# Kernel optimization log

Measured on AMD Instinct MI355X. Metric: run time of the kernel, lower is better.

Reference implementation:

```python
import jax, jax.numpy as jnp
from jax import lax
import numpy as np

N = 60000   # total nodes
B = 8       # graphs in batch
GS = N // B # nodes per graph
F = 384     # input node features
E = 600000  # edges
H = 6       # hiddenSize (hardcoded in source)
C = 10      # num_classes


def setup_inputs() -> dict:
    key = jax.random.key(0)
    ks = jax.random.split(key, 8)
    x = jax.random.normal(ks[0], (N, F), jnp.float32)
    src = jax.random.randint(ks[1], (E,), 0, N, jnp.int32)
    off = jax.random.randint(ks[2], (E,), 1, GS, jnp.int32)  # 1..GS-1 -> no self loops
    dst = (src // GS) * GS + (src % GS + off) % GS           # same-graph endpoint
    batch = jnp.arange(N, dtype=jnp.int32) // GS
    W1 = jax.random.normal(ks[3], (F, H), jnp.float32) * (1.0 / np.sqrt(F))
    b1 = jnp.zeros((H,), jnp.float32)
    W2 = jax.random.normal(ks[4], (H, C), jnp.float32) * (1.0 / np.sqrt(H))
    b2 = jnp.zeros((C,), jnp.float32)
    Wp1 = jax.random.normal(ks[5], (2 * H,), jnp.float32) * (1.0 / np.sqrt(2 * H))
    bp1 = jnp.zeros((), jnp.float32)
    Wp2 = jax.random.normal(ks[6], (2 * C,), jnp.float32) * (1.0 / np.sqrt(2 * C))
    bp2 = jnp.zeros((), jnp.float32)
    return dict(x=x, src=src, dst=dst, batch=batch, W1=W1, b1=b1, W2=W2, b2=b2,
                Wp1=Wp1, bp1=bp1, Wp2=Wp2, bp2=bp2)


def gcn_conv(x, src, dst, evalid, nvalid, W, b):
    # PyG GCNConv: h = x W; add remaining self-loops (weight 1); deg over dst;
    # norm = dinv[src]*dinv[dst]; aggregate to dst; + bias.
    n = x.shape[0]
    h = x @ W
    ef = evalid.astype(h.dtype)
    is_loop = evalid & (src == dst)
    has_loop = jax.ops.segment_sum(is_loop.astype(jnp.int32), dst, num_segments=n) > 0
    add_loop = (nvalid & ~has_loop).astype(h.dtype)
    deg = jax.ops.segment_sum(ef, dst, num_segments=n) + add_loop
    dinv = jnp.where(deg > 0, lax.rsqrt(jnp.maximum(deg, 1e-12)), 0.0)
    coef = ef * dinv[src] * dinv[dst]
    out = jax.ops.segment_sum(h[src] * coef[:, None], dst, num_segments=n)
    out = out + (add_loop * dinv * dinv)[:, None] * h
    return out + b


def edge_pool(x, src, dst, evalid, nvalid, Wp, bp):
    # PyG EdgePooling: raw = lin([x_src||x_dst]); score = softmax(raw, dst) + 0.5;
    # greedy contraction of edges by descending score; new_x = (sum over cluster) * score.
    n, f = x.shape
    raw = x[src] @ Wp[:f] + x[dst] @ Wp[f:] + bp                      # [E]
    rm = jnp.where(evalid, raw, -jnp.inf)
    m = jax.ops.segment_max(rm, dst, num_segments=n)
    m = jnp.where(jnp.isfinite(m), m, 0.0)
    ex = jnp.where(evalid, jnp.exp(raw - m[dst]), 0.0)
    s = jax.ops.segment_sum(ex, dst, num_segments=n)
    score = jnp.where(evalid, ex / jnp.where(s[dst] > 0, s[dst], 1.0), 0.0) + 0.5

    order = jnp.argsort(jnp.where(evalid, -score, jnp.inf))           # descending, invalid last

    def step(rem, edg):
        s_, d_, v_ = edg
        take = v_ & rem[s_] & rem[d_]
        rem = rem.at[s_].set(rem[s_] & ~take)
        rem = rem.at[d_].set(rem[d_] & ~take)
        return rem, take

    _, chosen_sorted = lax.scan(step, nvalid, (src[order], dst[order], evalid[order]))
    chosen = jnp.zeros_like(evalid).at[order].set(chosen_sorted)

    chf = chosen.astype(x.dtype)
    nonself = src != dst
    dead = jax.ops.segment_sum((chosen & nonself).astype(jnp.int32), dst, num_segments=n) > 0
    new_valid = nvalid & ~dead

    # merged feature: (x_src + x_dst) * score at slot src; unmatched: x * 1
    added = jnp.zeros_like(x).at[src].add((chf * nonself.astype(x.dtype))[:, None] * x[dst])
    scale = 1.0 + jnp.zeros((n,), x.dtype).at[src].add(chf * (score - 1.0))
    new_x = jnp.where(new_valid[:, None], (x + added) * scale[:, None], 0.0)

    # cluster map (dst of chosen edge -> src slot), remap + coalesce (dedup) edges
    merged_src = jnp.full((n,), -1, jnp.int32).at[dst].max(jnp.where(chosen, src, -1))
    cmap = jnp.where(merged_src >= 0, merged_src, jnp.arange(n, dtype=jnp.int32))
    ns, nd = cmap[src], cmap[dst]
    ns_k = jnp.where(evalid, ns, n)  # push invalid edges to the end
    order2 = jnp.lexsort((nd, ns_k))
    ss, dd = ns_k[order2], nd[order2]
    diff = (ss[1:] != ss[:-1]) | (dd[1:] != dd[:-1])
    first = jnp.concatenate([jnp.ones((1,), bool), diff])
    new_evalid = jnp.zeros_like(evalid).at[order2].set(first & evalid[order2])
    return new_x, ns, nd, new_evalid, new_valid


def _forward(x, src, dst, batch, W1, b1, W2, b2, Wp1, bp1, Wp2, bp2):
    evalid = jnp.ones((src.shape[0],), bool)
    nvalid = jnp.ones((x.shape[0],), bool)
    h = jax.nn.relu(gcn_conv(x, src, dst, evalid, nvalid, W1, b1))
    # dropout: identity in eval mode
    h, s1, d1, ev1, nv1 = edge_pool(h, src, dst, evalid, nvalid, Wp1, bp1)
    h = gcn_conv(h, s1, d1, ev1, nv1, W2, b2)
    h, s2, d2, ev2, nv2 = edge_pool(h, s1, d1, ev1, nv1, Wp2, bp2)
    nvf = nv2.astype(h.dtype)
    cnt = jax.ops.segment_sum(nvf, batch, num_segments=B)
    sm = jax.ops.segment_sum(h * nvf[:, None], batch, num_segments=B)
    g = sm / cnt[:, None]
    return jax.nn.log_softmax(g, axis=1)


def reference(x, src, dst, batch, W1, b1, W2, b2, Wp1, bp1, Wp2, bp2):
    return _forward(x, src, dst, batch, W1, b1, W2, b2, Wp1, bp1, Wp2, bp2)
```

## Files before the change

kernel.cpp:

```cpp
#include <hip/hip_runtime.h>
#include <math.h>

#define NN 60000
#define BB 8
#define GS 7500
#define FF 384
#define EE 600000
#define HH 6
#define CC 10
#define HT_BITS 20
#define HT_SIZE (1u << HT_BITS)
#define HT_MASK (HT_SIZE - 1u)
#define TPB 256
#define CAP 80000
#define REMW ((GS + 31) / 32)
#define GPAD 32
#define SCAN_B 1024
#define NBLK ((NN + SCAN_B - 1) / SCAN_B)
static_assert(NBLK <= 64, "scan2 assumes <=64 blocks");

static inline int ngrid(int n) { return (n + TPB - 1) / TPB; }

__device__ __forceinline__ unsigned long long mkprio(float sc, int e) {
  return (((unsigned long long)__float_as_uint(sc)) << 32) |
         (unsigned int)(~(unsigned int)e);
}

__global__ void k_mm1(const float* __restrict__ x, const float* __restrict__ W,
                      float* __restrict__ out) {
  __shared__ float Ws[FF * HH];
  for (int i = threadIdx.x; i < FF * HH; i += blockDim.x) Ws[i] = W[i];
  __syncthreads();
  int wave = threadIdx.x >> 6, lane = threadIdx.x & 63;
  int node = blockIdx.x * 4 + wave;
  if (node >= NN) return;
  const float* xr = x + (size_t)node * FF;
  float acc[HH] = {0.f, 0.f, 0.f, 0.f, 0.f, 0.f};
  for (int k = lane; k < FF; k += 64) {
    float xv = xr[k];
#pragma unroll
    for (int j = 0; j < HH; j++) acc[j] += xv * Ws[k * HH + j];
  }
#pragma unroll
  for (int j = 0; j < HH; j++) {
#pragma unroll
    for (int o = 32; o > 0; o >>= 1) acc[j] += __shfl_down(acc[j], o, 64);
  }
  if (lane == 0) {
#pragma unroll
    for (int j = 0; j < HH; j++) out[(size_t)node * HH + j] = acc[j];
  }
}

__global__ void k_prep(float* __restrict__ deg, unsigned char* __restrict__ hasloop,
                       int* __restrict__ gcntsA,
                       int* __restrict__ gcntsB, float* __restrict__ gsum,
                       float* __restrict__ gcnt, const unsigned char* __restrict__ nvin,
                       unsigned char* __restrict__ nvout, float* __restrict__ scale,
                       int* __restrict__ merged, int* __restrict__ partner,
                       unsigned long long* __restrict__ bestA,
                       unsigned long long* __restrict__ bestB,
                       unsigned char* __restrict__ remG) {
  int v = blockIdx.x * blockDim.x + threadIdx.x;
  if (v >= NN) return;
  deg[v] = 0.f;
  hasloop[v] = 0;
  unsigned char nvv = nvin ? nvin[v] : 1;
  nvout[v] = nvv;
  remG[v] = nvv;
  bestA[v] = 0ULL;
  bestB[v] = 0ULL;
  scale[v] = 1.0f;
  if (merged) merged[v] = -1;
  partner[v] = -1;
  if (v < BB * GPAD) { gcntsA[v] = 0; gcntsB[v] = 0; }
  if (v < BB * CC) gsum[v] = 0.f;
  if (v < BB) gcnt[v] = 0.f;
}

__global__ void k_deg(const int* __restrict__ src, const int* __restrict__ dst,
                      const unsigned char* __restrict__ ev, float* __restrict__ deg,
                      unsigned char* __restrict__ hasloop) {
  int e = blockIdx.x * blockDim.x + threadIdx.x;
  if (e >= EE) return;
  if (ev && !ev[e]) return;
  int d = dst[e];
  atomicAdd(&deg[d], 1.0f);
  if (src[e] == d) hasloop[d] = 1;
}

__global__ __launch_bounds__(1024) void k_scan1(const float* __restrict__ deg,
                                                int* __restrict__ rowstart,
                                                int* __restrict__ bsum) {
  __shared__ int tmp[SCAN_B];
  int t = threadIdx.x;
  int i = blockIdx.x * SCAN_B + t;
  int v = (i < NN) ? (int)deg[i] : 0;
  tmp[t] = v;
  __syncthreads();
  for (int o = 1; o < SCAN_B; o <<= 1) {
    int y = (t >= o) ? tmp[t - o] : 0;
    __syncthreads();
    tmp[t] += y;
    __syncthreads();
  }
  if (i < NN) rowstart[i] = tmp[t] - v;
  if (t == SCAN_B - 1) bsum[blockIdx.x] = tmp[t];
}

__global__ void k_scan2(int* __restrict__ bsum, int* __restrict__ rowstartNN) {
  int t = threadIdx.x;
  int v = (t < NBLK) ? bsum[t] : 0;
  int x = v;
#pragma unroll
  for (int o = 1; o < 64; o <<= 1) {
    int y = __shfl_up(x, o, 64);
    if (t >= o) x += y;
  }
  if (t < NBLK) bsum[t] = x - v;
  if (t == NBLK - 1) *rowstartNN = x;
}

__global__ void k_scan3(int* __restrict__ rowstart, const int* __restrict__ bsum,
                        int* __restrict__ fill, const float* __restrict__ deg,
                        const unsigned char* __restrict__ hasloop,
                        const unsigned char* __restrict__ nv, float* __restrict__ dinv,
                        unsigned char* __restrict__ addloop) {
  int i = blockIdx.x * blockDim.x + threadIdx.x;
  if (i >= NN) return;
  int r = rowstart[i] + bsum[i >> 10];
  rowstart[i] = r;
  fill[i] = r;
  int nvv = nv ? (int)nv[i] : 1;
  unsigned char al = (nvv && !hasloop[i]) ? 1 : 0;
  float d = deg[i] + (float)al;
  dinv[i] = d > 0.f ? 1.0f / sqrtf(fmaxf(d, 1e-12f)) : 0.f;
  addloop[i] = al;
}

__global__ void k_scatter(const int* __restrict__ src, const int* __restrict__ dst,
                          const unsigned char* __restrict__ ev, int* __restrict__ fill,
                          int* __restrict__ csrS, int* __restrict__ csrE) {
  int e = blockIdx.x * blockDim.x + threadIdx.x;
  if (e >= EE) return;
  if (ev && !ev[e]) return;
  int d = dst[e];
  int p = atomicAdd(&fill[d], 1);
  csrS[p] = src[e];
  csrE[p] = e;
}

template <int FD>
__global__ void k_agg_fin(const int* __restrict__ rowstart, const int* __restrict__ csrS,
                          const float* __restrict__ dinv, const unsigned char* __restrict__ addloop,
                          const float* __restrict__ h, const float* __restrict__ b,
                          float* __restrict__ out, int relu) {
  int v = blockIdx.x * blockDim.x + threadIdx.x;
  if (v >= NN) return;
  int b0 = rowstart[v], b1 = rowstart[v + 1];
  float acc[FD];
#pragma unroll
  for (int j = 0; j < FD; j++) acc[j] = 0.f;
  float dv = dinv[v];
  for (int i = b0; i < b1; i++) {
    int s = csrS[i];
    float c = dinv[s] * dv;
    const float* hr = h + (size_t)s * FD;
#pragma unroll
    for (int j = 0; j < FD; j++) acc[j] += hr[j] * c;
  }
  float cl = addloop[v] ? dv * dv : 0.f;
  const float* hv = h + (size_t)v * FD;
#pragma unroll
  for (int j = 0; j < FD; j++) {
    float o = acc[j] + cl * hv[j] + b[j];
    if (relu) o = fmaxf(o, 0.f);
    out[(size_t)v * FD + j] = o;
  }
}

__global__ void k_raw(const float* __restrict__ x, const int* __restrict__ src,
                      const int* __restrict__ dst, const unsigned char* __restrict__ ev,
                      const float* __restrict__ Wp, const float* __restrict__ bp,
                      float* __restrict__ raw, int fd) {
  int e = blockIdx.x * blockDim.x + threadIdx.x;
  if (e >= EE) return;
  if (ev && !ev[e]) return;
  int s = src[e], d = dst[e];
  float r = bp[0];
  for (int j = 0; j < fd; j++) r += x[(size_t)s * fd + j] * Wp[j];
  for (int j = 0; j < fd; j++) r += x[(size_t)d * fd + j] * Wp[fd + j];
  raw[e] = r;
}

__global__ void k_smscore(const int* __restrict__ rowstart, const int* __restrict__ csrS,
                          const int* __restrict__ csrE, const float* __restrict__ raw,
                          const unsigned char* __restrict__ remG, float* __restrict__ score,
                          unsigned long long* __restrict__ bestA) {
  int v = blockIdx.x * blockDim.x + threadIdx.x;
  if (v >= NN) return;
  int b0 = rowstart[v], b1 = rowstart[v + 1];
  if (b0 == b1) return;
  float m = -INFINITY;
  for (int i = b0; i < b1; i++) m = fmaxf(m, raw[csrE[i]]);
  float s = 0.f;
  for (int i = b0; i < b1; i++) s += expf(raw[csrE[i]] - m);
  if (!remG[v]) return;
  float sd = s > 0.f ? s : 1.0f;
  unsigned long long lb = 0ULL;
  for (int i = b0; i < b1; i++) {
    int sv = csrS[i];
    if (!remG[sv]) continue;
    int e = csrE[i];
    float sc = expf(raw[e] - m) / sd + 0.5f;
    score[e] = sc;
    unsigned long long p = mkprio(sc, e);
    if (p > lb) lb = p;
    if (sv != v && p > bestA[sv]) atomicMax(&bestA[sv], p);
  }
  if (lb > bestA[v]) atomicMax(&bestA[v], lb);
}

__global__ void k_r1sel(const int* __restrict__ src, const int* __restrict__ dst,
                        const float* __restrict__ score, const unsigned char* __restrict__ ev,
                        unsigned char* __restrict__ remG,
                        const unsigned long long* __restrict__ bestA,
                        unsigned long long* __restrict__ bestB,
                        unsigned char* __restrict__ chosen, ulonglong2* __restrict__ recs,
                        int* __restrict__ gcnts) {
  __shared__ int wcnt[TPB / 64][BB];
  __shared__ int bbase[BB];
  int e = blockIdx.x * blockDim.x + threadIdx.x;
  int w = threadIdx.x >> 6, lane = threadIdx.x & 63;
  int keep = 0, s = 0, d = 0, g = 0;
  unsigned long long p = 0;
  if (e < EE && (!ev || ev[e])) {
    s = src[e];
    d = dst[e];
    g = s / GS;
    if (remG[s] && remG[d]) {
      p = mkprio(score[e], e);
      if (bestA[s] == p && bestA[d] == p) {
        chosen[e] = 1;
        remG[s] = 0;
        remG[d] = 0;
      } else {
        keep = 1;
        bestB[s] = 0ULL;
        bestB[d] = 0ULL;
      }
    }
  }
  int myrank = 0;
#pragma unroll
  for (int gg = 0; gg < BB; gg++) {
    unsigned long long m = __ballot(keep && g == gg);
    if (keep && g == gg) myrank = __popcll(m & ((1ULL << lane) - 1ULL));
    if (lane == 0) wcnt[w][gg] = __popcll(m);
  }
  __syncthreads();
  if (threadIdx.x < BB) {
    int gg = threadIdx.x, tot = 0;
#pragma unroll
    for (int ww = 0; ww < TPB / 64; ww++) {
      int c = wcnt[ww][gg];
      wcnt[ww][gg] = tot;
      tot += c;
    }
    bbase[gg] = tot ? atomicAdd(&gcnts[gg * GPAD], tot) : 0;
  }
  __syncthreads();
  if (keep)
    recs[(size_t)g * CAP + bbase[g] + wcnt[w][g] + myrank] =
        make_ulonglong2(p, (((unsigned long long)(unsigned int)s) << 32) | (unsigned int)d);
}

__global__ void k_gpost(const ulonglong2* __restrict__ recs, const int* __restrict__ gcnts,
                        const unsigned char* __restrict__ remG,
                        unsigned long long* __restrict__ bestC, int* __restrict__ gcntsOut) {
  int g = blockIdx.y;
  if (blockIdx.x == 0 && threadIdx.x == 0) gcntsOut[g * GPAD] = 0;
  int n = gcnts[g * GPAD];
  const ulonglong2* lst = recs + (size_t)g * CAP;
  int stride = gridDim.x * blockDim.x;
  for (int i = blockIdx.x * blockDim.x + threadIdx.x; i < n; i += stride) {
    ulonglong2 r = lst[i];
    int s = (int)(r.y >> 32), d = (int)(r.y & 0xFFFFFFFFu);
    if (remG[s] && remG[d]) {
      if (r.x > bestC[s]) atomicMax(&bestC[s], r.x);
      if (d != s && r.x > bestC[d]) atomicMax(&bestC[d], r.x);
    }
  }
}

__global__ void k_gsel(const ulonglong2* __restrict__ recsIn, const int* __restrict__ gcntsIn,
                       unsigned char* __restrict__ remG,
                       const unsigned long long* __restrict__ bestC,
                       unsigned long long* __restrict__ bestN,
                       unsigned char* __restrict__ chosen, ulonglong2* __restrict__ recsOut,
                       int* __restrict__ gcntsOut) {
  int g = blockIdx.y;
  int n = gcntsIn[g * GPAD];
  const ulonglong2* lst = recsIn + (size_t)g * CAP;
  ulonglong2* outl = recsOut + (size_t)g * CAP;
  int lane = threadIdx.x & 63;
  int stride = gridDim.x * blockDim.x;
  for (int i = blockIdx.x * blockDim.x + threadIdx.x; i - lane < n; i += stride) {
    int keep = 0;
    ulonglong2 r;
    if (i < n) {
      r = lst[i];
      int s = (int)(r.y >> 32), d = (int)(r.y & 0xFFFFFFFFu);
      if (remG[s] && remG[d]) {
        if (bestC[s] == r.x && bestC[d] == r.x) {
          int e = (int)(~(unsigned int)(r.x & 0xFFFFFFFFu));
          chosen[e] = 1;
          remG[s] = 0;
          remG[d] = 0;
        } else {
          keep = 1;
          bestN[s] = 0ULL;
          bestN[d] = 0ULL;
        }
      }
    }
    unsigned long long m = __ballot(keep);
    int tot = __popcll(m);
    int pre = __popcll(m & ((1ULL << lane) - 1ULL));
    int b0 = 0;
    if (lane == 0 && tot) b0 = atomicAdd(&gcntsOut[g * GPAD], tot);
    b0 = __shfl(b0, 0, 64);
    if (keep) outl[b0 + pre] = r;
  }
}

__global__ __launch_bounds__(1024) void k_match_g(ulonglong2* __restrict__ recs0,
                                                  ulonglong2* __restrict__ recs1,
                                                  const int* __restrict__ gcnts,
                                                  const unsigned char* __restrict__ remG,
                                                  unsigned char* __restrict__ chosen) {
  __shared__ unsigned long long best[GS];
  __shared__ unsigned int remB[REMW];
  __shared__ int cnt_next;
  const int g = blockIdx.x;
  const int base = g * GS;
  const int t = threadIdx.x, nth = blockDim.x;
  const int lane = t & 63;

  for (int w = t; w < REMW; w += nth) {
    unsigned int bits = 0;
    int v0 = w * 32;
    if (v0 + 32 <= GS) {
      const unsigned int* p4 = (const unsigned int*)(remG + base + v0);
#pragma unroll
      for (int q = 0; q < 8; q++) {
        unsigned int x4 = p4[q];
        bits |= ((x4 & 1u) << (q * 4)) | (((x4 >> 8) & 1u) << (q * 4 + 1)) |
                (((x4 >> 16) & 1u) << (q * 4 + 2)) | (((x4 >> 24) & 1u) << (q * 4 + 3));
      }
    } else {
      for (int b = 0; b < 32; b++) {
        int v = v0 + b;
        if (v < GS) bits |= (remG[base + v] ? 1u : 0u) << b;
      }
    }
    remB[w] = bits;
  }
  for (int i = t; i < GS; i += nth) best[i] = 0ULL;
  __syncthreads();

  ulonglong2* bufs[2] = {recs0 + (size_t)g * CAP, recs1 + (size_t)g * CAP};
  int n = gcnts[g * GPAD];
  int cur = 0;
  int guard = 0;

  while (n > 0) {
    if (++guard > 100000) break;
    for (int i0 = 0; i0 < n; i0 += nth * 4) {
      ulonglong2 r[4];
      int have[4];
#pragma unroll
      for (int k = 0; k < 4; k++) {
        int i = i0 + t + k * nth;
        have[k] = i < n;
        if (have[k]) r[k] = bufs[cur][i];
      }
#pragma unroll
      for (int k = 0; k < 4; k++) {
        if (!have[k]) continue;
        int ls = (int)(r[k].y >> 32) - base, ld = (int)(r[k].y & 0xFFFFFFFFu) - base;
        if (((remB[ls >> 5] >> (ls & 31)) & 1u) && ((remB[ld >> 5] >> (ld & 31)) & 1u)) {
          atomicMax(&best[ls], r[k].x);
          if (ld != ls) atomicMax(&best[ld], r[k].x);
        }
      }
    }
    if (t == 0) cnt_next = 0;
    __syncthreads();
    for (int i0 = 0; i0 < n; i0 += nth * 4) {
      ulonglong2 r[4];
      int have[4];
#pragma unroll
      for (int k = 0; k < 4; k++) {
        int i = i0 + t + k * nth;
        have[k] = i < n;
        if (have[k]) r[k] = bufs[cur][i];
      }
#pragma unroll
      for (int k = 0; k < 4; k++) {
        int keep = 0;
        int ls = 0, ld = 0;
        if (have[k]) {
          ls = (int)(r[k].y >> 32) - base;
          ld = (int)(r[k].y & 0xFFFFFFFFu) - base;
          if (((remB[ls >> 5] >> (ls & 31)) & 1u) && ((remB[ld >> 5] >> (ld & 31)) & 1u)) {
            if (best[ls] == r[k].x && best[ld] == r[k].x) {
              int e = (int)(~(unsigned int)(r[k].x & 0xFFFFFFFFu));
              chosen[e] = 1;
              atomicAnd(&remB[ls >> 5], ~(1u << (ls & 31)));
              atomicAnd(&remB[ld >> 5], ~(1u << (ld & 31)));
            } else {
              keep = 1;
            }
          }
        }
        unsigned long long m = __ballot(keep);
        int tot = __popcll(m);
        int pre = __popcll(m & ((1ULL << lane) - 1ULL));
        int b0 = 0;
        if (lane == 0 && tot) b0 = atomicAdd(&cnt_next, tot);
        b0 = __shfl(b0, 0, 64);
        if (keep) bufs[cur ^ 1][b0 + pre] = r[k];
      }
    }
    __syncthreads();
    n = cnt_next;
    if (n < 4096) {
      for (int i = t; i < n; i += nth) {
        ulonglong2 r = bufs[cur ^ 1][i];
        best[(int)(r.y >> 32) - base] = 0ULL;
        best[(int)(r.y & 0xFFFFFFFFu) - base] = 0ULL;
      }
    } else {
      for (int i = t; i < GS; i += nth) best[i] = 0ULL;
    }
    __syncthreads();
    cur ^= 1;
  }
}

__global__ void k_pool_edge(const int* __restrict__ src, const int* __restrict__ dst,
                            const unsigned char* __restrict__ chosen, const float* __restrict__ score,
                            unsigned char* __restrict__ nvout, float* __restrict__ scale,
                            int* __restrict__ partner, int* __restrict__ merged) {
  int e = blockIdx.x * blockDim.x + threadIdx.x;
  if (e >= EE) return;
  if (!chosen[e]) return;
  int s = src[e], d = dst[e];
  scale[s] = score[e];
  if (merged) merged[d] = s;
  if (s != d) {
    nvout[d] = 0;
    partner[s] = d;
  }
}

__global__ void k_newx_mm2(const float* __restrict__ h1, const int* __restrict__ partner,
                           const float* __restrict__ scale, const unsigned char* __restrict__ nvout,
                           const float* __restrict__ W2, float* __restrict__ h2pre) {
  int v = blockIdx.x * blockDim.x + threadIdx.x;
  if (v >= NN) return;
  float sc = scale[v];
  int ok = nvout[v];
  int p = partner[v];
  float nx[HH];
#pragma unroll
  for (int j = 0; j < HH; j++) {
    float a = h1[(size_t)v * HH + j];
    if (p >= 0) a += h1[(size_t)p * HH + j];
    nx[j] = ok ? a * sc : 0.f;
  }
#pragma unroll
  for (int c = 0; c < CC; c++) {
    float a = 0.f;
#pragma unroll
    for (int j = 0; j < HH; j++) a += nx[j] * W2[j * CC + c];
    h2pre[(size_t)v * CC + c] = a;
  }
}

__device__ __forceinline__ unsigned int ht_hash(unsigned long long key) {
  return (unsigned int)((key * 0x9E3779B97F4A7C15ULL) >> 44) & HT_MASK;
}

__global__ void k_remap_ins(const int* __restrict__ src, const int* __restrict__ dst,
                            const int* __restrict__ merged, int* __restrict__ ns,
                            int* __restrict__ nd, unsigned long long* __restrict__ htab) {
  int e = blockIdx.x * blockDim.x + threadIdx.x;
  if (e >= EE) return;
  int s = src[e], d = dst[e];
  int ms = merged[s], md = merged[d];
  int a = ms >= 0 ? ms : s;
  int b = md >= 0 ? md : d;
  ns[e] = a;
  nd[e] = b;
  unsigned long long key =
      (unsigned long long)((((unsigned int)a) << 16) | (unsigned int)b);
  unsigned long long val = (key << 32) | (unsigned int)e;
  unsigned int h = ht_hash(key);
  for (;;) {
    unsigned long long curv = htab[h];
    if (curv == ~0ULL) {
      unsigned long long prev = atomicCAS(&htab[h], ~0ULL, val);
      if (prev == ~0ULL) break;
      curv = prev;
    }
    if ((curv >> 32) == key) {
      if ((curv & 0xFFFFFFFFULL) > (unsigned long long)(unsigned int)e)
        atomicMin(&htab[h], val);
      break;
    }
    h = (h + 1) & HT_MASK;
  }
}

__global__ void k_dedup_mark(const int* __restrict__ ns, const int* __restrict__ nd,
                             const unsigned long long* __restrict__ htab,
                             unsigned char* __restrict__ evout) {
  int e = blockIdx.x * blockDim.x + threadIdx.x;
  if (e >= EE) return;
  unsigned long long key =
      (unsigned long long)((((unsigned int)ns[e]) << 16) | (unsigned int)nd[e]);
  unsigned int h = ht_hash(key);
  for (;;) {
    unsigned long long curv = htab[h];
    if ((curv >> 32) == key) {
      evout[e] = ((curv & 0xFFFFFFFFULL) == (unsigned long long)(unsigned int)e) ? 1 : 0;
      return;
    }
    h = (h + 1) & HT_MASK;
  }
}

__global__ void k_newx_pool(const float* __restrict__ h2, const int* __restrict__ partner,
                            const float* __restrict__ scale, const unsigned char* __restrict__ nv,
                            float* __restrict__ gsum, float* __restrict__ gcnt) {
  int v = blockIdx.x * blockDim.x + threadIdx.x;
  int lane = threadIdx.x & 63;
  int b = (v < NN ? v : NN - 1) / GS;
  int active = (v < NN) && nv[v];
  float cnt = active ? 1.f : 0.f;
  float val[CC];
  if (active) {
    float sc = scale[v];
    int p = partner[v];
    for (int j = 0; j < CC; j++) {
      float a = h2[(size_t)v * CC + j];
      if (p >= 0) a += h2[(size_t)p * CC + j];
      val[j] = a * sc;
    }
  } else {
    for (int j = 0; j < CC; j++) val[j] = 0.f;
  }
  int b0 = __shfl(b, 0, 64);
  unsigned long long same = __ballot(b == b0);
  if (same == ~0ULL) {
    for (int o = 32; o > 0; o >>= 1) {
      cnt += __shfl_down(cnt, o, 64);
      for (int j = 0; j < CC; j++) val[j] += __shfl_down(val[j], o, 64);
    }
    if (lane == 0 && cnt > 0.f) {
      atomicAdd(&gcnt[b0], cnt);
      for (int j = 0; j < CC; j++) atomicAdd(&gsum[b0 * CC + j], val[j]);
    }
  } else if (active) {
    atomicAdd(&gcnt[b], cnt);
    for (int j = 0; j < CC; j++) atomicAdd(&gsum[b * CC + j], val[j]);
  }
}

__global__ void k_logsm(const float* __restrict__ gsum, const float* __restrict__ gcnt,
                        float* __restrict__ out) {
  int t = threadIdx.x;
  if (t >= BB) return;
  float gr[CC];
  float c = gcnt[t];
  float m = -INFINITY;
  for (int j = 0; j < CC; j++) {
    gr[j] = gsum[t * CC + j] / c;
    m = fmaxf(m, gr[j]);
  }
  float s = 0.f;
  for (int j = 0; j < CC; j++) s += expf(gr[j] - m);
  float l = logf(s);
  for (int j = 0; j < CC; j++) out[t * CC + j] = gr[j] - m - l;
}

extern "C" void kernel_launch(void* const* d_in, const int* in_sizes, int n_in,
                              void* d_out, int out_size, void* d_ws, size_t ws_size,
                              hipStream_t stream) {
  const float* x = (const float*)d_in[0];
  const int* src = (const int*)d_in[1];
  const int* dst = (const int*)d_in[2];
  const float* W1 = (const float*)d_in[4];
  const float* b1 = (const float*)d_in[5];
  const float* W2 = (const float*)d_in[6];
  const float* b2 = (const float*)d_in[7];
  const float* Wp1 = (const float*)d_in[8];
  const float* bp1 = (const float*)d_in[9];
  const float* Wp2 = (const float*)d_in[10];
  const float* bp2 = (const float*)d_in[11];
  float* out = (float*)d_out;

  char* wsb = (char*)d_ws;
  size_t off = 0;
  auto A = [&](size_t bytes) -> char* {
    char* r = wsb + off;
    off = (off + bytes + 255) & ~(size_t)255;
    return r;
  };
  float* h1pre = (float*)A((size_t)NN * HH * 4);
  float* h1out = (float*)A((size_t)NN * HH * 4);
  float* deg = (float*)A((size_t)NN * 4);
  float* dinv = (float*)A((size_t)NN * 4);
  unsigned char* hasloop = (unsigned char*)A(NN);
  unsigned char* addloop = (unsigned char*)A(NN);
  float* raw = (float*)A((size_t)EE * 4);
  float* score = (float*)A((size_t)EE * 4);
  unsigned char* chosen = (unsigned char*)A(EE);
  unsigned char* nv1 = (unsigned char*)A(NN);
  unsigned char* nv2 = (unsigned char*)A(NN);
  float* scale = (float*)A((size_t)NN * 4);
  int* partner = (int*)A((size_t)NN * 4);
  int* merged = (int*)A((size_t)NN * 4);
  int* ns = (int*)A((size_t)EE * 4);
  int* nd = (int*)A((size_t)EE * 4);
  unsigned char* ev1 = (unsigned char*)A(EE);
  unsigned long long* htab = (unsigned long long*)A((size_t)HT_SIZE * 8);
  float* h2pre = (float*)A((size_t)NN * CC * 4);
  float* h2out = (float*)A((size_t)NN * CC * 4);
  unsigned long long* bestA = (unsigned long long*)A((size_t)NN * 8);
  unsigned long long* bestB = (unsigned long long*)A((size_t)NN * 8);
  unsigned char* remG = (unsigned char*)A(NN);
  ulonglong2* recs0 = (ulonglong2*)A((size_t)BB * CAP * 16);
  ulonglong2* recs1 = (ulonglong2*)A((size_t)BB * CAP * 16);
  int* gcntsA = (int*)A((size_t)BB * GPAD * 4);
  int* gcntsB = (int*)A((size_t)BB * GPAD * 4);
  float* gsum = (float*)A((size_t)BB * CC * 4);
  float* gcnt = (float*)A((size_t)BB * 4);
  int* rowstart = (int*)A((size_t)(NN + 1) * 4);
  int* fill = (int*)A((size_t)NN * 4);
  int* bsum = (int*)A((size_t)64 * 4);
  int* csrS = (int*)A((size_t)EE * 4);
  int* csrE = (int*)A((size_t)EE * 4);
  (void)ws_size; (void)n_in; (void)in_sizes; (void)out_size;

  const int GE = ngrid(EE), GN = ngrid(NN);
  const dim3 RG(32, BB);

  hipMemsetAsync(htab, 0xFF, (size_t)HT_SIZE * 8, stream);
  hipLaunchKernelGGL(k_mm1, dim3((NN + 3) / 4), dim3(TPB), 0, stream, x, W1, h1pre);
  hipLaunchKernelGGL(k_prep, dim3(GN), dim3(TPB), 0, stream, deg, hasloop, gcntsA, gcntsB,
                     gsum, gcnt, (const unsigned char*)nullptr, nv1, scale, merged, partner, bestA, bestB, remG);
  hipLaunchKernelGGL(k_deg, dim3(GE), dim3(TPB), 0, stream, src, dst, (const unsigned char*)nullptr, deg, hasloop);
  hipLaunchKernelGGL(k_scan1, dim3(NBLK), dim3(SCAN_B), 0, stream, deg, rowstart, bsum);
  hipLaunchKernelGGL(k_scan2, dim3(1), dim3(64), 0, stream, bsum, rowstart + NN);
  hipLaunchKernelGGL(k_scan3, dim3(GN), dim3(TPB), 0, stream, rowstart, bsum, fill, deg, hasloop,
                     (const unsigned char*)nullptr, dinv, addloop);
  hipLaunchKernelGGL(k_scatter, dim3(GE), dim3(TPB), 0, stream, src, dst, (const unsigned char*)nullptr, fill, csrS, csrE);
  hipLaunchKernelGGL(k_agg_fin<HH>, dim3(GN), dim3(TPB), 0, stream, rowstart, csrS, dinv, addloop, h1pre, b1, h1out, 1);

  hipLaunchKernelGGL(k_raw, dim3(GE), dim3(TPB), 0, stream, h1out, src, dst, (const unsigned char*)nullptr, Wp1, bp1, raw, HH);
  hipMemsetAsync(chosen, 0, (size_t)EE, stream);
  hipLaunchKernelGGL(k_smscore, dim3(GN), dim3(TPB), 0, stream, rowstart, csrS, csrE, raw, remG, score, bestA);
  hipLaunchKernelGGL(k_r1sel, dim3(GE), dim3(TPB), 0, stream, src, dst, score, (const unsigned char*)nullptr, remG, bestA, bestB, chosen, recs0, gcntsA);
  hipLaunchKernelGGL(k_gpost, RG, dim3(TPB), 0, stream, recs0, gcntsA, remG, bestB, gcntsB);
  hipLaunchKernelGGL(k_gsel, RG, dim3(TPB), 0, stream, recs0, gcntsA, remG, bestB, bestA, chosen, recs1, gcntsB);
  hipLaunchKernelGGL(k_gpost, RG, dim3(TPB), 0, stream, recs1, gcntsB, remG, bestA, gcntsA);
  hipLaunchKernelGGL(k_gsel, RG, dim3(TPB), 0, stream, recs1, gcntsB, remG, bestA, bestB, chosen, recs0, gcntsA);
  hipLaunchKernelGGL(k_gpost, RG, dim3(TPB), 0, stream, recs0, gcntsA, remG, bestB, gcntsB);
  hipLaunchKernelGGL(k_gsel, RG, dim3(TPB), 0, stream, recs0, gcntsA, remG, bestB, bestA, chosen, recs1, gcntsB);
  hipLaunchKernelGGL(k_gpost, RG, dim3(TPB), 0, stream, recs1, gcntsB, remG, bestA, gcntsA);
  hipLaunchKernelGGL(k_gsel, RG, dim3(TPB), 0, stream, recs1, gcntsB, remG, bestA, bestB, chosen, recs0, gcntsA);
  hipLaunchKernelGGL(k_gpost, RG, dim3(TPB), 0, stream, recs0, gcntsA, remG, bestB, gcntsB);
  hipLaunchKernelGGL(k_gsel, RG, dim3(TPB), 0, stream, recs0, gcntsA, remG, bestB, bestA, chosen, recs1, gcntsB);
  hipLaunchKernelGGL(k_match_g, dim3(BB), dim3(1024), 0, stream, recs1, recs0, gcntsB, remG, chosen);
  hipLaunchKernelGGL(k_pool_edge, dim3(GE), dim3(TPB), 0, stream, src, dst, chosen, score, nv1, scale, partner, merged);
  hipLaunchKernelGGL(k_newx_mm2, dim3(GN), dim3(TPB), 0, stream, h1out, partner, scale, nv1, W2, h2pre);
  hipLaunchKernelGGL(k_remap_ins, dim3(GE), dim3(TPB), 0, stream, src, dst, merged, ns, nd, htab);
  hipLaunchKernelGGL(k_dedup_mark, dim3(GE), dim3(TPB), 0, stream, ns, nd, htab, ev1);

  hipLaunchKernelGGL(k_prep, dim3(GN), dim3(TPB), 0, stream, deg, hasloop, gcntsA, gcntsB,
                     gsum, gcnt, (const unsigned char*)nv1, nv2, scale, (int*)nullptr, partner, bestA, bestB, remG);
  hipLaunchKernelGGL(k_deg, dim3(GE), dim3(TPB), 0, stream, ns, nd, (const unsigned char*)ev1, deg, hasloop);
  hipLaunchKernelGGL(k_scan1, dim3(NBLK), dim3(SCAN_B), 0, stream, deg, rowstart, bsum);
  hipLaunchKernelGGL(k_scan2, dim3(1), dim3(64), 0, stream, bsum, rowstart + NN);
  hipLaunchKernelGGL(k_scan3, dim3(GN), dim3(TPB), 0, stream, rowstart, bsum, fill, deg, hasloop,
                     (const unsigned char*)nv1, dinv, addloop);
  hipLaunchKernelGGL(k_scatter, dim3(GE), dim3(TPB), 0, stream, ns, nd, (const unsigned char*)ev1, fill, csrS, csrE);
  hipLaunchKernelGGL(k_agg_fin<CC>, dim3(GN), dim3(TPB), 0, stream, rowstart, csrS, dinv, addloop, h2pre, b2, h2out, 0);

  hipLaunchKernelGGL(k_raw, dim3(GE), dim3(TPB), 0, stream, h2out, ns, nd, (const unsigned char*)ev1, Wp2, bp2, raw, CC);
  hipMemsetAsync(chosen, 0, (size_t)EE, stream);
  hipLaunchKernelGGL(k_smscore, dim3(GN), dim3(TPB), 0, stream, rowstart, csrS, csrE, raw, remG, score, bestA);
  hipLaunchKernelGGL(k_r1sel, dim3(GE), dim3(TPB), 0, stream, ns, nd, score, (const unsigned char*)ev1, remG, bestA, bestB, chosen, recs0, gcntsA);
  hipLaunchKernelGGL(k_gpost, RG, dim3(TPB), 0, stream, recs0, gcntsA, remG, bestB, gcntsB);
  hipLaunchKernelGGL(k_gsel, RG, dim3(TPB), 0, stream, recs0, gcntsA, remG, bestB, bestA, chosen, recs1, gcntsB);
  hipLaunchKernelGGL(k_gpost, RG, dim3(TPB), 0, stream, recs1, gcntsB, remG, bestA, gcntsA);
  hipLaunchKernelGGL(k_gsel, RG, dim3(TPB), 0, stream, recs1, gcntsB, remG, bestA, bestB, chosen, recs0, gcntsA);
  hipLaunchKernelGGL(k_gpost, RG, dim3(TPB), 0, stream, recs0, gcntsA, remG, bestB, gcntsB);
  hipLaunchKernelGGL(k_gsel, RG, dim3(TPB), 0, stream, recs0, gcntsA, remG, bestB, bestA, chosen, recs1, gcntsB);
  hipLaunchKernelGGL(k_gpost, RG, dim3(TPB), 0, stream, recs1, gcntsB, remG, bestA, gcntsA);
  hipLaunchKernelGGL(k_gsel, RG, dim3(TPB), 0, stream, recs1, gcntsB, remG, bestA, bestB, chosen, recs0, gcntsA);
  hipLaunchKernelGGL(k_gpost, RG, dim3(TPB), 0, stream, recs0, gcntsA, remG, bestB, gcntsB);
  hipLaunchKernelGGL(k_gsel, RG, dim3(TPB), 0, stream, recs0, gcntsA, remG, bestB, bestA, chosen, recs1, gcntsB);
  hipLaunchKernelGGL(k_match_g, dim3(BB), dim3(1024), 0, stream, recs1, recs0, gcntsB, remG, chosen);
  hipLaunchKernelGGL(k_pool_edge, dim3(GE), dim3(TPB), 0, stream, ns, nd, chosen, score, nv2, scale, partner, (int*)nullptr);

  hipLaunchKernelGGL(k_newx_pool, dim3(GN), dim3(TPB), 0, stream, h2out, partner, scale, nv2, gsum, gcnt);
  hipLaunchKernelGGL(k_logsm, dim3(1), dim3(64), 0, stream, gsum, gcnt, out);
}
```

Measured before the change: 1.469 ms.

## Fuse greedy-matching post/select rounds via round-tagged priorities and fold scan2 into scan3

Puts a round number into the high bits of each best-priority value, so each round can publish next-round maxima while it selects, without resetting arrays. This merges the separate post and select kernels into one k_gselpost per round, using three rotating counters. Also folds the single-block scan2 into scan3 (each block redoes the 64-entry wave scan) and moves clearing of the chosen array into k_raw instead of a memset. The goal is fewer launches and fewer passes over the record lists, at the cost of packing score bits and edge index into 51 bits, which assumes fewer than 2^20 edges.

New measurement: 1.707 ms. 1.16x slower.

```diff
diff --git a/kernel.cpp b/kernel.cpp
--- a/kernel.cpp
+++ b/kernel.cpp
@@ -17,13 +17,18 @@
 #define GPAD 32
 #define SCAN_B 1024
 #define NBLK ((NN + SCAN_B - 1) / SCAN_B)
-static_assert(NBLK <= 64, "scan2 assumes <=64 blocks");
+static_assert(NBLK <= 64, "scan3 wave-scan assumes <=64 blocks");
+static_assert(EE < (1 << 20), "tag tie-break assumes e < 2^20");
 
 static inline int ngrid(int n) { return (n + TPB - 1) / TPB; }
 
 __device__ __forceinline__ unsigned long long mkprio(float sc, int e) {
   return (((unsigned long long)__float_as_uint(sc)) << 32) |
          (unsigned int)(~(unsigned int)e);
+}
+__device__ __forceinline__ unsigned long long mktag(unsigned long long round,
+                                                    unsigned long long prio) {
+  return (round << 51) | ((prio >> 32) << 20) | ((unsigned int)prio & 0xFFFFFu);
 }
 
 __global__ void k_mm1(const float* __restrict__ x, const float* __restrict__ W,
@@ -53,8 +58,8 @@
 }
 
 __global__ void k_prep(float* __restrict__ deg, unsigned char* __restrict__ hasloop,
-                       int* __restrict__ gcntsA,
-                       int* __restrict__ gcntsB, float* __restrict__ gsum,
+                       int* __restrict__ gcntsA, int* __restrict__ gcntsB,
+                       int* __restrict__ gcntsC, float* __restrict__ gsum,
                        float* __restrict__ gcnt, const unsigned char* __restrict__ nvin,
                        unsigned char* __restrict__ nvout, float* __restrict__ scale,
                        int* __restrict__ merged, int* __restrict__ partner,
@@ -73,7 +78,7 @@
   scale[v] = 1.0f;
   if (merged) merged[v] = -1;
   partner[v] = -1;
-  if (v < BB * GPAD) { gcntsA[v] = 0; gcntsB[v] = 0; }
+  if (v < BB * GPAD) { gcntsA[v] = 0; gcntsB[v] = 0; gcntsC[v] = 0; }
   if (v < BB * CC) gsum[v] = 0.f;
   if (v < BB) gcnt[v] = 0.f;
 }
@@ -108,29 +113,32 @@
   if (t == SCAN_B - 1) bsum[blockIdx.x] = tmp[t];
 }
 
-__global__ void k_scan2(int* __restrict__ bsum, int* __restrict__ rowstartNN) {
-  int t = threadIdx.x;
-  int v = (t < NBLK) ? bsum[t] : 0;
-  int x = v;
-#pragma unroll
-  for (int o = 1; o < 64; o <<= 1) {
-    int y = __shfl_up(x, o, 64);
-    if (t >= o) x += y;
-  }
-  if (t < NBLK) bsum[t] = x - v;
-  if (t == NBLK - 1) *rowstartNN = x;
-}
-
 __global__ void k_scan3(int* __restrict__ rowstart, const int* __restrict__ bsum,
                         int* __restrict__ fill, const float* __restrict__ deg,
                         const unsigned char* __restrict__ hasloop,
                         const unsigned char* __restrict__ nv, float* __restrict__ dinv,
                         unsigned char* __restrict__ addloop) {
-  int i = blockIdx.x * blockDim.x + threadIdx.x;
+  __shared__ int offs[64];
+  __shared__ int total;
+  int t = threadIdx.x;
+  if (t < 64) {
+    int v = (t < NBLK) ? bsum[t] : 0;
+    int x = v;
+#pragma unroll
+    for (int o = 1; o < 64; o <<= 1) {
+      int y = __shfl_up(x, o, 64);
+      if (t >= o) x += y;
+    }
+    offs[t] = x - v;
+    if (t == 63) total = x;
+  }
+  __syncthreads();
+  int i = blockIdx.x * blockDim.x + t;
   if (i >= NN) return;
-  int r = rowstart[i] + bsum[i >> 10];
+  int r = rowstart[i] + offs[i >> 10];
   rowstart[i] = r;
   fill[i] = r;
+  if (i == NN - 1) rowstart[NN] = total;
   int nvv = nv ? (int)nv[i] : 1;
   unsigned char al = (nvv && !hasloop[i]) ? 1 : 0;
   float d = deg[i] + (float)al;
@@ -182,9 +190,10 @@
 __global__ void k_raw(const float* __restrict__ x, const int* __restrict__ src,
                       const int* __restrict__ dst, const unsigned char* __restrict__ ev,
                       const float* __restrict__ Wp, const float* __restrict__ bp,
-                      float* __restrict__ raw, int fd) {
+                      float* __restrict__ raw, unsigned char* __restrict__ chosen, int fd) {
   int e = blockIdx.x * blockDim.x + threadIdx.x;
   if (e >= EE) return;
+  chosen[e] = 0;
   if (ev && !ev[e]) return;
   int s = src[e], d = dst[e];
   float r = bp[0];
@@ -216,9 +225,15 @@
     score[e] = sc;
     unsigned long long p = mkprio(sc, e);
     if (p > lb) lb = p;
-    if (sv != v && p > bestA[sv]) atomicMax(&bestA[sv], p);
-  }
-  if (lb > bestA[v]) atomicMax(&bestA[v], lb);
+    if (sv != v) {
+      unsigned long long t1 = mktag(1, p);
+      if (t1 > bestA[sv]) atomicMax(&bestA[sv], t1);
+    }
+  }
+  if (lb) {
+    unsigned long long t1 = mktag(1, lb);
+    if (t1 > bestA[v]) atomicMax(&bestA[v], t1);
+  }
 }
 
 __global__ void k_r1sel(const int* __restrict__ src, const int* __restrict__ dst,
@@ -240,14 +255,16 @@
     g = s / GS;
     if (remG[s] && remG[d]) {
       p = mkprio(score[e], e);
-      if (bestA[s] == p && bestA[d] == p) {
+      unsigned long long t1 = mktag(1, p);
+      if (bestA[s] == t1 && bestA[d] == t1) {
         chosen[e] = 1;
         remG[s] = 0;
         remG[d] = 0;
       } else {
         keep = 1;
-        bestB[s] = 0ULL;
-        bestB[d] = 0ULL;
+        unsigned long long t2 = mktag(2, p);
+        atomicMax(&bestB[s], t2);
+        if (d != s) atomicMax(&bestB[d], t2);
       }
     }
   }
@@ -275,52 +292,37 @@
         make_ulonglong2(p, (((unsigned long long)(unsigned int)s) << 32) | (unsigned int)d);
 }
 
-__global__ void k_gpost(const ulonglong2* __restrict__ recs, const int* __restrict__ gcnts,
-                        const unsigned char* __restrict__ remG,
-                        unsigned long long* __restrict__ bestC, int* __restrict__ gcntsOut) {
+__global__ void k_gselpost(const ulonglong2* __restrict__ recsIn, const int* __restrict__ cntIn,
+                           unsigned char* __restrict__ remG,
+                           const unsigned long long* __restrict__ bestIn,
+                           unsigned long long* __restrict__ bestOut,
+                           unsigned char* __restrict__ chosen, ulonglong2* __restrict__ recsOut,
+                           int* __restrict__ cntOut, int* __restrict__ cntZero,
+                           unsigned long long rnd) {
   int g = blockIdx.y;
-  if (blockIdx.x == 0 && threadIdx.x == 0) gcntsOut[g * GPAD] = 0;
-  int n = gcnts[g * GPAD];
-  const ulonglong2* lst = recs + (size_t)g * CAP;
-  int stride = gridDim.x * blockDim.x;
-  for (int i = blockIdx.x * blockDim.x + threadIdx.x; i < n; i += stride) {
-    ulonglong2 r = lst[i];
-    int s = (int)(r.y >> 32), d = (int)(r.y & 0xFFFFFFFFu);
-    if (remG[s] && remG[d]) {
-      if (r.x > bestC[s]) atomicMax(&bestC[s], r.x);
-      if (d != s && r.x > bestC[d]) atomicMax(&bestC[d], r.x);
-    }
-  }
-}
-
-__global__ void k_gsel(const ulonglong2* __restrict__ recsIn, const int* __restrict__ gcntsIn,
-                       unsigned char* __restrict__ remG,
-                       const unsigned long long* __restrict__ bestC,
-                       unsigned long long* __restrict__ bestN,
-                       unsigned char* __restrict__ chosen, ulonglong2* __restrict__ recsOut,
-                       int* __restrict__ gcntsOut) {
-  int g = blockIdx.y;
-  int n = gcntsIn[g * GPAD];
+  if (blockIdx.x == 0 && threadIdx.x == 0) cntZero[g * GPAD] = 0;
+  int n = cntIn[g * GPAD];
   const ulonglong2* lst = recsIn + (size_t)g * CAP;
   ulonglong2* outl = recsOut + (size_t)g * CAP;
   int lane = threadIdx.x & 63;
   int stride = gridDim.x * blockDim.x;
   for (int i = blockIdx.x * blockDim.x + threadIdx.x; i - lane < n; i += stride) {
     int keep = 0;
+    int s = 0, d = 0;
     ulonglong2 r;
     if (i < n) {
       r = lst[i];
-      int s = (int)(r.y >> 32), d = (int)(r.y & 0xFFFFFFFFu);
+      s = (int)(r.y >> 32);
+      d = (int)(r.y & 0xFFFFFFFFu);
       if (remG[s] && remG[d]) {
-        if (bestC[s] == r.x && bestC[d] == r.x) {
+        unsigned long long tc = mktag(rnd, r.x);
+        if (bestIn[s] == tc && bestIn[d] == tc) {
           int e = (int)(~(unsigned int)(r.x & 0xFFFFFFFFu));
           chosen[e] = 1;
           remG[s] = 0;
           remG[d] = 0;
         } else {
           keep = 1;
-          bestN[s] = 0ULL;
-          bestN[d] = 0ULL;
         }
       }
     }
@@ -328,9 +330,14 @@
     int tot = __popcll(m);
     int pre = __popcll(m & ((1ULL << lane) - 1ULL));
     int b0 = 0;
-    if (lane == 0 && tot) b0 = atomicAdd(&gcntsOut[g * GPAD], tot);
+    if (lane == 0 && tot) b0 = atomicAdd(&cntOut[g * GPAD], tot);
     b0 = __shfl(b0, 0, 64);
-    if (keep) outl[b0 + pre] = r;
+    if (keep) {
+      outl[b0 + pre] = r;
+      unsigned long long tn = mktag(rnd + 1, r.x);
+      atomicMax(&bestOut[s], tn);
+      if (d != s) atomicMax(&bestOut[d], tn);
+    }
   }
 }
 
@@ -646,6 +653,7 @@
   ulonglong2* recs1 = (ulonglong2*)A((size_t)BB * CAP * 16);
   int* gcntsA = (int*)A((size_t)BB * GPAD * 4);
   int* gcntsB = (int*)A((size_t)BB * GPAD * 4);
+  int* gcntsC = (int*)A((size_t)BB * GPAD * 4);
   float* gsum = (float*)A((size_t)BB * CC * 4);
   float* gcnt = (float*)A((size_t)BB * 4);
   int* rowstart = (int*)A((size_t)(NN + 1) * 4);
@@ -660,61 +668,47 @@
 
   hipMemsetAsync(htab, 0xFF, (size_t)HT_SIZE * 8, stream);
   hipLaunchKernelGGL(k_mm1, dim3((NN + 3) / 4), dim3(TPB), 0, stream, x, W1, h1pre);
-  hipLaunchKernelGGL(k_prep, dim3(GN), dim3(TPB), 0, stream, deg, hasloop, gcntsA, gcntsB,
+  hipLaunchKernelGGL(k_prep, dim3(GN), dim3(TPB), 0, stream, deg, hasloop, gcntsA, gcntsB, gcntsC,
                      gsum, gcnt, (const unsigned char*)nullptr, nv1, scale, merged, partner, bestA, bestB, remG);
   hipLaunchKernelGGL(k_deg, dim3(GE), dim3(TPB), 0, stream, src, dst, (const unsigned char*)nullptr, deg, hasloop);
   hipLaunchKernelGGL(k_scan1, dim3(NBLK), dim3(SCAN_B), 0, stream, deg, rowstart, bsum);
-  hipLaunchKernelGGL(k_scan2, dim3(1), dim3(64), 0, stream, bsum, rowstart + NN);
   hipLaunchKernelGGL(k_scan3, dim3(GN), dim3(TPB), 0, stream, rowstart, bsum, fill, deg, hasloop,
                      (const unsigned char*)nullptr, dinv, addloop);
   hipLaunchKernelGGL(k_scatter, dim3(GE), dim3(TPB), 0, stream, src, dst, (const unsigned char*)nullptr, fill, csrS, csrE);
   hipLaunchKernelGGL(k_agg_fin<HH>, dim3(GN), dim3(TPB), 0, stream, rowstart, csrS, dinv, addloop, h1pre, b1, h1out, 1);
 
-  hipLaunchKernelGGL(k_raw, dim3(GE), dim3(TPB), 0, stream, h1out, src, dst, (const unsigned char*)nullptr, Wp1, bp1, raw, HH);
-  hipMemsetAsync(chosen, 0, (size_t)EE, stream);
+  hipLaunchKernelGGL(k_raw, dim3(GE), dim3(TPB), 0, stream, h1out, src, dst, (const unsigned char*)nullptr, Wp1, bp1, raw, chosen, HH);
   hipLaunchKernelGGL(k_smscore, dim3(GN), dim3(TPB), 0, stream, rowstart, csrS, csrE, raw, remG, score, bestA);
   hipLaunchKernelGGL(k_r1sel, dim3(GE), dim3(TPB), 0, stream, src, dst, score, (const unsigned char*)nullptr, remG, bestA, bestB, chosen, recs0, gcntsA);
-  hipLaunchKernelGGL(k_gpost, RG, dim3(TPB), 0, stream, recs0, gcntsA, remG, bestB, gcntsB);
-  hipLaunchKernelGGL(k_gsel, RG, dim3(TPB), 0, stream, recs0, gcntsA, remG, bestB, bestA, chosen, recs1, gcntsB);
-  hipLaunchKernelGGL(k_gpost, RG, dim3(TPB), 0, stream, recs1, gcntsB, remG, bestA, gcntsA);
-  hipLaunchKernelGGL(k_gsel, RG, dim3(TPB), 0, stream, recs1, gcntsB, remG, bestA, bestB, chosen, recs0, gcntsA);
-  hipLaunchKernelGGL(k_gpost, RG, dim3(TPB), 0, stream, recs0, gcntsA, remG, bestB, gcntsB);
-  hipLaunchKernelGGL(k_gsel, RG, dim3(TPB), 0, stream, recs0, gcntsA, remG, bestB, bestA, chosen, recs1, gcntsB);
-  hipLaunchKernelGGL(k_gpost, RG, dim3(TPB), 0, stream, recs1, gcntsB, remG, bestA, gcntsA);
-  hipLaunchKernelGGL(k_gsel, RG, dim3(TPB), 0, stream, recs1, gcntsB, remG, bestA, bestB, chosen, recs0, gcntsA);
-  hipLaunchKernelGGL(k_gpost, RG, dim3(TPB), 0, stream, recs0, gcntsA, remG, bestB, gcntsB);
-  hipLaunchKernelGGL(k_gsel, RG, dim3(TPB), 0, stream, recs0, gcntsA, remG, bestB, bestA, chosen, recs1, gcntsB);
-  hipLaunchKernelGGL(k_match_g, dim3(BB), dim3(1024), 0, stream, recs1, recs0, gcntsB, remG, chosen);
+  hipLaunchKernelGGL(k_gselpost, RG, dim3(TPB), 0, stream, recs0, gcntsA, remG, bestB, bestA, chosen, recs1, gcntsB, gcntsC, 2ULL);
+  hipLaunchKernelGGL(k_gselpost, RG, dim3(TPB), 0, stream, recs1, gcntsB, remG, bestA, bestB, chosen, recs0, gcntsC, gcntsA, 3ULL);
+  hipLaunchKernelGGL(k_gselpost, RG, dim3(TPB), 0, stream, recs0, gcntsC, remG, bestB, bestA, chosen, recs1, gcntsA, gcntsB, 4ULL);
+  hipLaunchKernelGGL(k_gselpost, RG, dim3(TPB), 0, stream, recs1, gcntsA, remG, bestA, bestB, chosen, recs0, gcntsB, gcntsC, 5ULL);
+  hipLaunchKernelGGL(k_gselpost, RG, dim3(TPB), 0, stream, recs0, gcntsB, remG, bestB, bestA, chosen, recs1, gcntsC, gcntsA, 6ULL);
+  hipLaunchKernelGGL(k_match_g, dim3(BB), dim3(1024), 0, stream, recs1, recs0, gcntsC, remG, chosen);
   hipLaunchKernelGGL(k_pool_edge, dim3(GE), dim3(TPB), 0, stream, src, dst, chosen, score, nv1, scale, partner, merged);
   hipLaunchKernelGGL(k_newx_mm2, dim3(GN), dim3(TPB), 0, stream, h1out, partner, scale, nv1, W2, h2pre);
   hipLaunchKernelGGL(k_remap_ins, dim3(GE), dim3(TPB), 0, stream, src, dst, merged, ns, nd, htab);
   hipLaunchKernelGGL(k_dedup_mark, dim3(GE), dim3(TPB), 0, stream, ns, nd, htab, ev1);
 
-  hipLaunchKernelGGL(k_prep, dim3(GN), dim3(TPB), 0, stream, deg, hasloop, gcntsA, gcntsB,
+  hipLaunchKernelGGL(k_prep, dim3(GN), dim3(TPB), 0, stream, deg, hasloop, gcntsA, gcntsB, gcntsC,
                      gsum, gcnt, (const unsigned char*)nv1, nv2, scale, (int*)nullptr, partner, bestA, bestB, remG);
   hipLaunchKernelGGL(k_deg, dim3(GE), dim3(TPB), 0, stream, ns, nd, (const unsigned char*)ev1, deg, hasloop);
   hipLaunchKernelGGL(k_scan1, dim3(NBLK), dim3(SCAN_B), 0, stream, deg, rowstart, bsum);
-  hipLaunchKernelGGL(k_scan2, dim3(1), dim3(64), 0, stream, bsum, rowstart + NN);
   hipLaunchKernelGGL(k_scan3, dim3(GN), dim3(TPB), 0, stream, rowstart, bsum, fill, deg, hasloop,
                      (const unsigned char*)nv1, dinv, addloop);
   hipLaunchKernelGGL(k_scatter, dim3(GE), dim3(TPB), 0, stream, ns, nd, (const unsigned char*)ev1, fill, csrS, csrE);
   hipLaunchKernelGGL(k_agg_fin<CC>, dim3(GN), dim3(TPB), 0, stream, rowstart, csrS, dinv, addloop, h2pre, b2, h2out, 0);
 
-  hipLaunchKernelGGL(k_raw, dim3(GE), dim3(TPB), 0, stream, h2out, ns, nd, (const unsigned char*)ev1, Wp2, bp2, raw, CC);
-  hipMemsetAsync(chosen, 0, (size_t)EE, stream);
+  hipLaunchKernelGGL(k_raw, dim3(GE), dim3(TPB), 0, stream, h2out, ns, nd, (const unsigned char*)ev1, Wp2, bp2, raw, chosen, CC);
   hipLaunchKernelGGL(k_smscore, dim3(GN), dim3(TPB), 0, stream, rowstart, csrS, csrE, raw, remG, score, bestA);
   hipLaunchKernelGGL(k_r1sel, dim3(GE), dim3(TPB), 0, stream, ns, nd, score, (const unsigned char*)ev1, remG, bestA, bestB, chosen, recs0, gcntsA);
-  hipLaunchKernelGGL(k_gpost, RG, dim3(TPB), 0, stream, recs0, gcntsA, remG, bestB, gcntsB);
-  hipLaunchKernelGGL(k_gsel, RG, dim3(TPB), 0, stream, recs0, gcntsA, remG, bestB, bestA, chosen, recs1, gcntsB);
-  hipLaunchKernelGGL(k_gpost, RG, dim3(TPB), 0, stream, recs1, gcntsB, remG, bestA, gcntsA);
-  hipLaunchKernelGGL(k_gsel, RG, dim3(TPB), 0, stream, recs1, gcntsB, remG, bestA, bestB, chosen, recs0, gcntsA);
-  hipLaunchKernelGGL(k_gpost, RG, dim3(TPB), 0, stream, recs0, gcntsA, remG, bestB, gcntsB);
-  hipLaunchKernelGGL(k_gsel, RG, dim3(TPB), 0, stream, recs0, gcntsA, remG, bestB, bestA, chosen, recs1, gcntsB);
-  hipLaunchKernelGGL(k_gpost, RG, dim3(TPB), 0, stream, recs1, gcntsB, remG, bestA, gcntsA);
-  hipLaunchKernelGGL(k_gsel, RG, dim3(TPB), 0, stream, recs1, gcntsB, remG, bestA, bestB, chosen, recs0, gcntsA);
-  hipLaunchKernelGGL(k_gpost, RG, dim3(TPB), 0, stream, recs0, gcntsA, remG, bestB, gcntsB);
-  hipLaunchKernelGGL(k_gsel, RG, dim3(TPB), 0, stream, recs0, gcntsA, remG, bestB, bestA, chosen, recs1, gcntsB);
-  hipLaunchKernelGGL(k_match_g, dim3(BB), dim3(1024), 0, stream, recs1, recs0, gcntsB, remG, chosen);
+  hipLaunchKernelGGL(k_gselpost, RG, dim3(TPB), 0, stream, recs0, gcntsA, remG, bestB, bestA, chosen, recs1, gcntsB, gcntsC, 2ULL);
+  hipLaunchKernelGGL(k_gselpost, RG, dim3(TPB), 0, stream, recs1, gcntsB, remG, bestA, bestB, chosen, recs0, gcntsC, gcntsA, 3ULL);
+  hipLaunchKernelGGL(k_gselpost, RG, dim3(TPB), 0, stream, recs0, gcntsC, remG, bestB, bestA, chosen, recs1, gcntsA, gcntsB, 4ULL);
+  hipLaunchKernelGGL(k_gselpost, RG, dim3(TPB), 0, stream, recs1, gcntsA, remG, bestA, bestB, chosen, recs0, gcntsB, gcntsC, 5ULL);
+  hipLaunchKernelGGL(k_gselpost, RG, dim3(TPB), 0, stream, recs0, gcntsB, remG, bestB, bestA, chosen, recs1, gcntsC, gcntsA, 6ULL);
+  hipLaunchKernelGGL(k_match_g, dim3(BB), dim3(1024), 0, stream, recs1, recs0, gcntsC, remG, chosen);
   hipLaunchKernelGGL(k_pool_edge, dim3(GE), dim3(TPB), 0, stream, ns, nd, chosen, score, nv2, scale, partner, (int*)nullptr);
 
   hipLaunchKernelGGL(k_newx_pool, dim3(GN), dim3(TPB), 0, stream, h2out, partner, scale, nv2, gsum, gcnt);
```
